# Kernel tuning notes

Measured on AMD Instinct MI355X. Metric: run time of the kernel, lower is better.

Reference implementation:

```python
import jax, jax.numpy as jnp
import numpy as np
from functools import partial

D = 512      # world_state_dim
M = 1000     # memory_size
H = 8        # attention heads
DH = D // H  # head dim
EPS = 1e-5


def _layernorm(x, g, b):
    mu = jnp.mean(x, axis=-1, keepdims=True)
    var = jnp.mean((x - mu) ** 2, axis=-1, keepdims=True)
    return (x - mu) * jax.lax.rsqrt(var + EPS) * g + b


def setup_inputs() -> dict:
    key = jax.random.key(0)
    ks = jax.random.split(key, 24)
    B = 8192
    w = lambda k, shp: (jax.random.normal(k, shp, dtype=jnp.float32) * 0.02)
    inp = {
        "observations": jax.random.normal(ks[0], (B, D), dtype=jnp.float32),
        "ego_motion": jax.random.normal(ks[1], (B, 16), dtype=jnp.float32),
        "world_memory": jax.random.normal(ks[2], (M, D), dtype=jnp.float32) * 0.1,
        # encoder: Linear(D,D) -> ReLU -> LN(D) -> Linear(D,D)
        "enc_w1": w(ks[3], (D, D)), "enc_b1": jnp.zeros((D,), jnp.float32),
        "enc_g": jnp.ones((D,), jnp.float32), "enc_beta": jnp.zeros((D,), jnp.float32),
        "enc_w2": w(ks[4], (D, D)), "enc_b2": jnp.zeros((D,), jnp.float32),
        # multihead attention in/out projections
        "wq": w(ks[5], (D, D)), "bq": jnp.zeros((D,), jnp.float32),
        "wk": w(ks[6], (D, D)), "bk": jnp.zeros((D,), jnp.float32),
        "wv": w(ks[7], (D, D)), "bv": jnp.zeros((D,), jnp.float32),
        "wo": w(ks[8], (D, D)), "bo": jnp.zeros((D,), jnp.float32),
        # transition: Linear(D+16,D) -> ReLU -> LN(D) -> Linear(D,D)
        "tr_w1": w(ks[9], (D, D + 16)), "tr_b1": jnp.zeros((D,), jnp.float32),
        "tr_g": jnp.ones((D,), jnp.float32), "tr_beta": jnp.zeros((D,), jnp.float32),
        "tr_w2": w(ks[10], (D, D)), "tr_b2": jnp.zeros((D,), jnp.float32),
        # quality head: Linear(D,128) -> ReLU -> Linear(128,1) -> Sigmoid
        "q_w1": w(ks[11], (128, D)), "q_b1": jnp.zeros((128,), jnp.float32),
        "q_w2": w(ks[12], (1, 128)), "q_b2": jnp.zeros((1,), jnp.float32),
        # random slots for memory-bank scatter-EMA update (replaces torch.randint)
        "update_indices": jax.random.randint(ks[13], (B,), 0, M, dtype=jnp.int32),
    }
    return inp


def _forward_core(observations, ego_motion, world_memory,
                  enc_w1, enc_b1, enc_g, enc_beta, enc_w2, enc_b2,
                  wq, bq, wk, bk, wv, bv, wo, bo,
                  tr_w1, tr_b1, tr_g, tr_beta, tr_w2, tr_b2,
                  q_w1, q_b1, q_w2, q_b2):
    B = observations.shape[0]
    # world_encoder
    h = jax.nn.relu(observations @ enc_w1.T + enc_b1)
    encoded = _layernorm(h, enc_g, enc_beta) @ enc_w2.T + enc_b2  # [B, D]
    # cross-attention: one query per batch row over shared memory bank
    q = (encoded @ wq.T + bq).reshape(B, H, DH)
    k = (world_memory @ wk.T + bk).reshape(M, H, DH)  # shared across batch
    v = (world_memory @ wv.T + bv).reshape(M, H, DH)
    scores = jnp.einsum("bhd,mhd->bhm", q, k) / jnp.sqrt(jnp.float32(DH))
    attn = jax.nn.softmax(scores, axis=-1)              # [B, H, M]
    ctx = jnp.einsum("bhm,mhd->bhd", attn, v).reshape(B, D)
    memory_states = ctx @ wo.T + bo
    # fuse + transition
    fused = 0.7 * encoded + 0.3 * memory_states
    x = jnp.concatenate([fused, ego_motion], axis=-1)   # [B, D+16]
    h2 = jax.nn.relu(x @ tr_w1.T + tr_b1)
    next_state = _layernorm(h2, tr_g, tr_beta) @ tr_w2.T + tr_b2  # [B, D]
    # quality head
    qh = jax.nn.relu(next_state @ q_w1.T + q_b1)
    quality = jax.nn.sigmoid(qh @ q_w2.T + q_b2)        # [B, 1]
    mem_weights = jnp.mean(attn, axis=1)                # [B, M] avg over heads
    return next_state, quality, mem_weights


def _update_memory_bank(world_memory, next_state, quality, update_indices):
    # Sequential scatter-EMA, faithful to the torch loop (duplicates compound).
    mask = quality[:, 0] > 0.7

    def step(mem, inp):
        idx, st, m = inp
        row = mem[idx]
        new_row = jnp.where(m, 0.9 * row + 0.1 * st, row)
        return mem.at[idx].set(new_row), None

    updated, _ = jax.lax.scan(step, world_memory, (update_indices, next_state, mask))
    return updated


@jax.jit
def reference(observations, ego_motion, world_memory,
              enc_w1, enc_b1, enc_g, enc_beta, enc_w2, enc_b2,
              wq, bq, wk, bk, wv, bv, wo, bo,
              tr_w1, tr_b1, tr_g, tr_beta, tr_w2, tr_b2,
              q_w1, q_b1, q_w2, q_b2, update_indices):
    next_state, quality, mem_weights = _forward_core(
        observations, ego_motion, world_memory,
        enc_w1, enc_b1, enc_g, enc_beta, enc_w2, enc_b2,
        wq, bq, wk, bk, wv, bv, wo, bo,
        tr_w1, tr_b1, tr_g, tr_beta, tr_w2, tr_b2,
        q_w1, q_b1, q_w2, q_b2)
    updated_memory = _update_memory_bank(world_memory, next_state, quality, update_indices)
    return next_state, quality, updated_memory
```

## Files before the change

kernel.cpp:

```cpp
#include <hip/hip_runtime.h>

#define B_ 8192
#define D_ 512
#define M_ 1000
#define H_ 8
#define LOG2E 1.4426950408889634f

typedef unsigned short u16;
typedef __attribute__((ext_vector_type(8))) short bf16x8;
typedef __attribute__((ext_vector_type(4))) float f32x4;

__device__ __forceinline__ float bf2f(u16 u) {
    union { unsigned u; float f; } c; c.u = ((unsigned)u) << 16; return c.f;
}
__device__ __forceinline__ u16 f2bf(float f) {
    union { float f; unsigned u; } c; c.f = f;
    unsigned r = (c.u + 0x7fffu + ((c.u >> 16) & 1u)) >> 16;
    return (u16)r;
}
__device__ __forceinline__ unsigned f2bf_fast_u(float f) {
    union { float f; unsigned u; } c; c.f = f;
    return (c.u + 0x8000u) >> 16;
}
__device__ __forceinline__ float wave_sum(float v) {
#pragma unroll
    for (int off = 32; off > 0; off >>= 1) v += __shfl_xor(v, off);
    return v;
}

template<bool RELU, bool WF32, bool VTOUT>
__device__ __forceinline__ void gemm_core(
    int bx, int by, u16* As, u16* Bs,
    const u16* __restrict__ A0, const u16* __restrict__ A1,
    const u16* __restrict__ A2, int lda0, int lda1, int lda2,
    const u16* __restrict__ W0, const u16* __restrict__ W1,
    const u16* __restrict__ W2, int ldw0, int ldw1, int ldw2,
    int kb1, int kb2,
    const float* __restrict__ bias, float bscale, float cscale,
    float* __restrict__ Cf, u16* __restrict__ Cb, u16* __restrict__ VT,
    int M, int N, int K, int ldc)
{
    const int m0 = by * 64, n0 = bx * 64;
    if (m0 >= M || n0 >= N) return;
    const int t = threadIdx.x, w = t >> 6, l = t & 63;
    const int wm = (w >> 1) * 32, wn = (w & 1) * 32;
    const int li = l & 15, quad = l >> 4;

    f32x4 acc[2][2];
#pragma unroll
    for (int i = 0; i < 2; ++i)
#pragma unroll
        for (int j = 0; j < 2; ++j) acc[i][j] = (f32x4){0.f, 0.f, 0.f, 0.f};

    for (int k0 = 0; k0 < K; k0 += 64) {
        const u16* Ab; const u16* Wb; int ldab, ldwb, ko;
        if (k0 < kb1)      { Ab = A0; ldab = lda0; Wb = W0; ldwb = ldw0; ko = k0; }
        else if (k0 < kb2) { Ab = A1; ldab = lda1; Wb = W1; ldwb = ldw1; ko = k0 - kb1; }
        else               { Ab = A2; ldab = lda2; Wb = W2; ldwb = ldw2; ko = k0 - kb2; }
#pragma unroll
        for (int i = 0; i < 2; ++i) {
            const int rl = w * 16 + i * 8 + (l >> 3);
            const int ck = (l & 7) ^ (rl & 7);
            int ga = m0 + rl; ga = ga < M ? ga : M - 1;
            __builtin_amdgcn_global_load_lds(
                (const __attribute__((address_space(1))) void*)(Ab + (size_t)ga * ldab + ko + ck * 8),
                (__attribute__((address_space(3))) void*)(As + (w * 16 + i * 8) * 64),
                16, 0, 0);
        }
#pragma unroll
        for (int i = 0; i < 2; ++i) {
            const int rl = w * 16 + i * 8 + (l >> 3);
            const int ck = (l & 7) ^ (rl & 7);
            int gb = n0 + rl; gb = gb < N ? gb : N - 1;
            __builtin_amdgcn_global_load_lds(
                (const __attribute__((address_space(1))) void*)(Wb + (size_t)gb * ldwb + ko + ck * 8),
                (__attribute__((address_space(3))) void*)(Bs + (w * 16 + i * 8) * 64),
                16, 0, 0);
        }
        __syncthreads();
#pragma unroll
        for (int ks = 0; ks < 2; ++ks) {
            const int ch = ks * 4 + quad;
            bf16x8 af[2], bfr[2];
#pragma unroll
            for (int mt = 0; mt < 2; ++mt) {
                const int r = wm + mt * 16 + li;
                af[mt] = *(const bf16x8*)(As + r * 64 + ((ch ^ (r & 7)) * 8));
            }
#pragma unroll
            for (int nt = 0; nt < 2; ++nt) {
                const int r = wn + nt * 16 + li;
                bfr[nt] = *(const bf16x8*)(Bs + r * 64 + ((ch ^ (r & 7)) * 8));
            }
#pragma unroll
            for (int mt = 0; mt < 2; ++mt)
#pragma unroll
                for (int nt = 0; nt < 2; ++nt)
                    acc[mt][nt] = __builtin_amdgcn_mfma_f32_16x16x32_bf16(
                        af[mt], bfr[nt], acc[mt][nt], 0, 0, 0);
        }
        __syncthreads();
    }

    float bv[2];
#pragma unroll
    for (int nt = 0; nt < 2; ++nt) bv[nt] = bias[n0 + wn + nt * 16 + li] * bscale;
#pragma unroll
    for (int mt = 0; mt < 2; ++mt) {
        const int row0 = m0 + wm + mt * 16 + quad * 4;
#pragma unroll
        for (int nt = 0; nt < 2; ++nt) {
            const int col = n0 + wn + nt * 16 + li;
            if (VTOUT && col >= 512) {
                ushort4 pk;
                u16 pv[4];
#pragma unroll
                for (int r = 0; r < 4; ++r) {
                    float v = acc[mt][nt][r] * cscale + bv[nt];
                    pv[r] = (row0 + r < M_) ? f2bf(v) : (u16)0;
                }
                pk.x = pv[0]; pk.y = pv[1]; pk.z = pv[2]; pk.w = pv[3];
                *(ushort4*)(VT + (size_t)(col - 512) * 1024 + row0) = pk;
            } else {
#pragma unroll
                for (int r = 0; r < 4; ++r) {
                    const int row = row0 + r;
                    if (row >= M) continue;
                    float v = acc[mt][nt][r] * cscale + bv[nt];
                    if (RELU) v = fmaxf(v, 0.f);
                    Cb[(size_t)row * ldc + col] = f2bf(v);
                    if (WF32) Cf[(size_t)row * ldc + col] = v;
                }
            }
        }
    }
}

template<bool RELU, bool WF32>
__launch_bounds__(256)
__global__ void mgemm(const u16* __restrict__ A0, const u16* __restrict__ A1,
                      const u16* __restrict__ A2, int lda0, int lda1, int lda2,
                      const u16* __restrict__ W0, const u16* __restrict__ W1,
                      const u16* __restrict__ W2, int ldw0, int ldw1, int ldw2,
                      int kb1, int kb2,
                      const float* __restrict__ bias, float bscale, float cscale,
                      float* __restrict__ Cf, u16* __restrict__ Cb,
                      int M, int N, int K, int ldc)
{
    __shared__ u16 As[64 * 64];
    __shared__ u16 Bs[64 * 64];
    gemm_core<RELU, WF32, false>(blockIdx.x, blockIdx.y, As, Bs,
                                 A0, A1, A2, lda0, lda1, lda2,
                                 W0, W1, W2, ldw0, ldw1, ldw2, kb1, kb2,
                                 bias, bscale, cscale, Cf, Cb, nullptr, M, N, K, ldc);
}

__launch_bounds__(256)
__global__ void megagemm(const u16* __restrict__ obs_bf, const u16* __restrict__ w_enc1,
                         const float* __restrict__ enc_b1, u16* __restrict__ hbuf,
                         const u16* __restrict__ wmem_bf, const u16* __restrict__ w_k,
                         const float* __restrict__ bkv, u16* __restrict__ KVbuf,
                         u16* __restrict__ VTb,
                         const u16* __restrict__ w_q, const u16* __restrict__ w_tr1,
                         const u16* __restrict__ w_e2t, const u16* __restrict__ w_wot,
                         u16* __restrict__ w_qe, u16* __restrict__ w_ae,
                         u16* __restrict__ w_co)
{
    __shared__ u16 As[64 * 64];
    __shared__ u16 Bs[64 * 64];
    const int bx = blockIdx.x, by = blockIdx.y;
    if (blockIdx.z == 0) {
        gemm_core<true, false, false>(bx, by, As, Bs,
            obs_bf, obs_bf, obs_bf, 512, 512, 512,
            w_enc1, w_enc1, w_enc1, 512, 512, 512, 512, 512,
            enc_b1, 1.f, 1.f, nullptr, hbuf, nullptr, B_, 512, 512, 512);
    } else {
        if (by < 16) {
            gemm_core<false, false, true>(bx, by, As, Bs,
                wmem_bf, wmem_bf, wmem_bf, 512, 512, 512,
                w_k, w_k, w_k, 512, 512, 512, 512, 512,
                bkv, 1.f, 1.f, nullptr, KVbuf, VTb, 1024, 1024, 512, 1024);
        } else if (by < 24) {
            gemm_core<false, false, false>(bx, by - 16, As, Bs,
                w_q, w_q, w_q, 512, 512, 512,
                w_e2t, w_e2t, w_e2t, 512, 512, 512, 512, 512,
                bkv, 0.f, 1.0f, nullptr, w_qe, nullptr, 512, 512, 512, 512);
        } else if (by < 32) {
            gemm_core<false, false, false>(bx, by - 24, As, Bs,
                w_tr1, w_tr1, w_tr1, 576, 576, 576,
                w_e2t, w_e2t, w_e2t, 512, 512, 512, 512, 512,
                bkv, 0.f, 0.7f, nullptr, w_ae, nullptr, 512, 512, 512, 512);
        } else if (by < 40) {
            gemm_core<false, false, false>(bx, by - 32, As, Bs,
                w_tr1, w_tr1, w_tr1, 576, 576, 576,
                w_wot, w_wot, w_wot, 512, 512, 512, 512, 512,
                bkv, 0.f, 0.3f, nullptr, w_co, nullptr, 512, 512, 512, 512);
        }
    }
}

#define PADK 72

__launch_bounds__(256, 3)
__global__ void attn_kernel(const u16* __restrict__ Q, const u16* __restrict__ KV,
                            const u16* __restrict__ VT, u16* __restrict__ ctx)
{
    __shared__ u16 Ks[2][64 * 64];
    __shared__ u16 Vs[2][64 * 64];
    __shared__ u16 P[4 * 32 * PADK];
    const int t = threadIdx.x, w = t >> 6, l = t & 63;
    const int h = blockIdx.y;
    const int q0 = blockIdx.x * 128 + w * 32;
    u16* Pw = P + w * (32 * PADK);
    const int li = l & 15, quad = l >> 4;

    bf16x8 aq[2][2];
#pragma unroll
    for (int qnt = 0; qnt < 2; ++qnt)
#pragma unroll
        for (int ks = 0; ks < 2; ++ks) {
            const int row = q0 + qnt * 16 + li;
            aq[qnt][ks] = *(const bf16x8*)(Q + (size_t)row * 512 + h * 64 + ks * 32 + quad * 8);
        }

    bf16x8 ones;
#pragma unroll
    for (int i = 0; i < 8; ++i) ones[i] = (short)0x3F80;

    f32x4 oacc[2][4];
    f32x4 lacc[2];
#pragma unroll
    for (int mt = 0; mt < 2; ++mt) {
        lacc[mt] = (f32x4){0.f, 0.f, 0.f, 0.f};
#pragma unroll
        for (int nt = 0; nt < 4; ++nt) oacc[mt][nt] = (f32x4){0.f, 0.f, 0.f, 0.f};
    }

    auto stage = [&](int kc, int buf) {
#pragma unroll
        for (int i = 0; i < 2; ++i) {
            const int f = i * 256 + t;
            const int r = f >> 3;
            const int ck = (f & 7) ^ (r & 7);
            __builtin_amdgcn_global_load_lds(
                (const __attribute__((address_space(1))) void*)(KV + (size_t)(kc + r) * 1024 + h * 64 + ck * 8),
                (__attribute__((address_space(3))) void*)(&Ks[buf][f * 8]),
                16, 0, 0);
        }
#pragma unroll
        for (int i = 0; i < 2; ++i) {
            const int f = i * 256 + t;
            const int r = f >> 3;
            const int ck = (f & 7) ^ (r & 7);
            __builtin_amdgcn_global_load_lds(
                (const __attribute__((address_space(1))) void*)(VT + (size_t)(h * 64 + r) * 1024 + kc + ck * 8),
                (__attribute__((address_space(3))) void*)(&Vs[buf][f * 8]),
                16, 0, 0);
        }
    };

    stage(0, 0);
    for (int ic = 0; ic < 16; ++ic) {
        const int kc = ic * 64;
        __syncthreads();
        if (ic < 15) stage(kc + 64, (ic + 1) & 1);
        const u16* ksb = &Ks[ic & 1][0];
        const u16* vsb = &Vs[ic & 1][0];

        f32x4 s[4][2];
#pragma unroll
        for (int kmt = 0; kmt < 4; ++kmt)
#pragma unroll
            for (int qnt = 0; qnt < 2; ++qnt) s[kmt][qnt] = (f32x4){0.f, 0.f, 0.f, 0.f};
#pragma unroll
        for (int ks = 0; ks < 2; ++ks) {
            const int ch = ks * 4 + quad;
            bf16x8 bk[4];
#pragma unroll
            for (int kmt = 0; kmt < 4; ++kmt) {
                const int key = kmt * 16 + li;
                bk[kmt] = *(const bf16x8*)(ksb + key * 64 + ((ch ^ (key & 7)) * 8));
            }
#pragma unroll
            for (int kmt = 0; kmt < 4; ++kmt)
#pragma unroll
                for (int qnt = 0; qnt < 2; ++qnt)
                    s[kmt][qnt] = __builtin_amdgcn_mfma_f32_16x16x32_bf16(
                        bk[kmt], aq[qnt][ks], s[kmt][qnt], 0, 0, 0);
        }
        if (kc == 960) {
#pragma unroll
            for (int kmt = 2; kmt < 4; ++kmt)
#pragma unroll
                for (int r = 0; r < 4; ++r) {
                    const int key_local = kmt * 16 + quad * 4 + r;
                    if (960 + key_local >= M_) {
                        s[kmt][0][r] = -3.0e38f;
                        s[kmt][1][r] = -3.0e38f;
                    }
                }
        }
#pragma unroll
        for (int kmt = 0; kmt < 4; ++kmt)
#pragma unroll
            for (int qnt = 0; qnt < 2; ++qnt) {
                const unsigned b0 = f2bf_fast_u(exp2f(s[kmt][qnt][0]));
                const unsigned b1 = f2bf_fast_u(exp2f(s[kmt][qnt][1]));
                const unsigned b2w = f2bf_fast_u(exp2f(s[kmt][qnt][2]));
                const unsigned b3 = f2bf_fast_u(exp2f(s[kmt][qnt][3]));
                const int off = (qnt * 16 + li) * PADK + kmt * 16 + quad * 4;
                *(uint2*)(Pw + off) = make_uint2(b0 | (b1 << 16), b2w | (b3 << 16));
            }
#pragma unroll
        for (int ks = 0; ks < 2; ++ks) {
            const int ch = ks * 4 + quad;
            bf16x8 ap[2];
#pragma unroll
            for (int mt = 0; mt < 2; ++mt)
                ap[mt] = *(const bf16x8*)(Pw + (mt * 16 + li) * PADK + ch * 8);
#pragma unroll
            for (int mt = 0; mt < 2; ++mt)
                lacc[mt] = __builtin_amdgcn_mfma_f32_16x16x32_bf16(
                    ap[mt], ones, lacc[mt], 0, 0, 0);
#pragma unroll
            for (int nt = 0; nt < 4; ++nt) {
                const int dh = nt * 16 + li;
                const bf16x8 bvv = *(const bf16x8*)(vsb + dh * 64 + ((ch ^ (dh & 7)) * 8));
#pragma unroll
                for (int mt = 0; mt < 2; ++mt)
                    oacc[mt][nt] = __builtin_amdgcn_mfma_f32_16x16x32_bf16(
                        ap[mt], bvv, oacc[mt][nt], 0, 0, 0);
            }
        }
    }

#pragma unroll
    for (int mt = 0; mt < 2; ++mt)
#pragma unroll
        for (int r = 0; r < 4; ++r) {
            const int row = q0 + mt * 16 + quad * 4 + r;
            const float inv = 1.0f / lacc[mt][r];
#pragma unroll
            for (int nt = 0; nt < 4; ++nt)
                ctx[(size_t)row * 512 + h * 64 + nt * 16 + li] = f2bf(oacc[mt][nt][r] * inv);
        }
}

__launch_bounds__(256)
__global__ void ln_bf(u16* __restrict__ X, const float* __restrict__ g,
                      const float* __restrict__ be, int rows)
{
    const int row = blockIdx.x * 4 + (threadIdx.x >> 6);
    const int lane = threadIdx.x & 63;
    if (row >= rows) return;
    u16* p = X + (size_t)row * 512 + lane * 8;
    uint4 d = *(const uint4*)p;
    const unsigned dd[4] = {d.x, d.y, d.z, d.w};
    float v[8];
#pragma unroll
    for (int i = 0; i < 4; ++i) {
        v[2 * i]     = bf2f((u16)(dd[i] & 0xffffu));
        v[2 * i + 1] = bf2f((u16)(dd[i] >> 16));
    }
    float s = 0.f;
#pragma unroll
    for (int i = 0; i < 8; ++i) s += v[i];
    s = wave_sum(s);
    const float mu = s * (1.0f / 512.0f);
    float vs = 0.f;
#pragma unroll
    for (int i = 0; i < 8; ++i) { v[i] -= mu; vs += v[i] * v[i]; }
    vs = wave_sum(vs);
    const float r = rsqrtf(vs * (1.0f / 512.0f) + 1e-5f);
    const float* gp = g + lane * 8;
    const float* bp = be + lane * 8;
    unsigned o[4];
#pragma unroll
    for (int i = 0; i < 4; ++i) {
        const u16 lo = f2bf(v[2 * i] * r * gp[2 * i] + bp[2 * i]);
        const u16 hi = f2bf(v[2 * i + 1] * r * gp[2 * i + 1] + bp[2 * i + 1]);
        o[i] = (unsigned)lo | ((unsigned)hi << 16);
    }
    *(uint4*)p = make_uint4(o[0], o[1], o[2], o[3]);
}

__launch_bounds__(256)
__global__ void prep_all(const float* enc_w1, const float* wk_f, const float* wv_f,
                         const float* tr_w2, const float* q_w1, const float* wq,
                         const float* tr_w1, const float* enc_w2, const float* wo,
                         const float* obs, const float* wmem, const float* ego,
                         const float* bk, const float* bvv, const float* bq,
                         const float* enc_b2, const float* trb1, const float* bo,
                         u16* w_enc1, u16* w_k, u16* w_v, u16* w_tr2, u16* w_qh,
                         u16* w_q, u16* w_tr1, u16* w_e2t, u16* w_wot,
                         u16* obs_bf, u16* wmem_bf, u16* ego64,
                         float* bkv, float* bqe, float* btr)
{
    __shared__ float tl[64][65];
    const int seg = blockIdx.y;
    const int t = threadIdx.x;
    const int bx = blockIdx.x;

    if (seg <= 5) {
        const float* s; u16* d; int n; float sc = 1.0f;
        switch (seg) {
            case 0: s = enc_w1; d = w_enc1; n = 262144; break;
            case 1: s = wk_f;   d = w_k;    n = 262144; break;
            case 2: s = wv_f;   d = w_v;    n = 262144; break;
            case 3: s = tr_w2;  d = w_tr2;  n = 262144; break;
            case 4: s = q_w1;   d = w_qh;   n = 65536;  break;
            default: s = wq;    d = w_q;    n = 262144; sc = 0.125f * LOG2E; break;
        }
        const int i0 = (bx * 256 + t) * 4;
        if (i0 + 3 < n) {
            const float4 v = *(const float4*)(s + i0);
            ushort4 o;
            o.x = f2bf(v.x * sc); o.y = f2bf(v.y * sc);
            o.z = f2bf(v.z * sc); o.w = f2bf(v.w * sc);
            *(ushort4*)(d + i0) = o;
        }
    } else if (seg == 6) {
#pragma unroll
        for (int k = 0; k < 4; ++k) {
            const int i = (bx * 256 + t) * 4 + k;
            if (i < 294912) {
                const int r = i / 576, c = i - r * 576;
                w_tr1[i] = (c < 528) ? f2bf(tr_w1[r * 528 + c]) : (u16)0;
            }
        }
    } else if (seg <= 8) {
        if (bx >= 64) return;
        const float* S = (seg == 7) ? enc_w2 : wo;
        u16* D = (seg == 7) ? w_e2t : w_wot;
        const int r0 = (bx >> 3) * 64, c0 = (bx & 7) * 64;
#pragma unroll
        for (int i = 0; i < 16; ++i) {
            const int idx = t + i * 256;
            tl[idx >> 6][idx & 63] = S[(size_t)(r0 + (idx >> 6)) * 512 + c0 + (idx & 63)];
        }
        __syncthreads();
#pragma unroll
        for (int i = 0; i < 16; ++i) {
            const int idx = t + i * 256;
            const int c = idx >> 6, r = idx & 63;
            D[(size_t)(c0 + c) * 512 + r0 + r] = f2bf(tl[r][c]);
        }
    } else if (seg == 9) {
        const int nth = gridDim.x * 256;
        for (int i = bx * 256 + t; i < B_ * 512 / 4; i += nth) {
            const float4 v = ((const float4*)obs)[i];
            ushort4 o;
            o.x = f2bf(v.x); o.y = f2bf(v.y); o.z = f2bf(v.z); o.w = f2bf(v.w);
            ((ushort4*)obs_bf)[i] = o;
        }
    } else if (seg == 10) {
        const int nth = gridDim.x * 256;
        for (int i = bx * 256 + t; i < M_ * 512 / 4; i += nth) {
            const float4 v = ((const float4*)wmem)[i];
            ushort4 o;
            o.x = f2bf(v.x); o.y = f2bf(v.y); o.z = f2bf(v.z); o.w = f2bf(v.w);
            ((ushort4*)wmem_bf)[i] = o;
        }
    } else if (seg == 11) {
        const int nth = gridDim.x * 256;
        for (int i = bx * 256 + t; i < B_ * 64; i += nth) {
            const int b = i >> 6, j = i & 63;
            ego64[(size_t)b * 64 + j] = (j < 16) ? f2bf(ego[b * 16 + j]) : (u16)0;
        }
        const int tid = bx * 256 + t;
        if (tid < 1024) bkv[tid] = (tid < 512) ? bk[tid] : bvv[tid - 512];
    } else {
        if (bx >= 128) return;
        const int i = bx * 4 + (t >> 6);
        const int lane = t & 63;
        float s = 0.f;
        if (seg == 12) {
            const float* wr = wq + (size_t)i * 512 + lane * 8;
#pragma unroll
            for (int j = 0; j < 8; ++j) s += wr[j] * enc_b2[lane * 8 + j];
            s = wave_sum(s);
            if (lane == 0) bqe[i] = 0.125f * LOG2E * (bq[i] + s);
        } else {
            const float* wr = tr_w1 + (size_t)i * 528 + lane * 8;
#pragma unroll
            for (int j = 0; j < 8; ++j)
                s += wr[j] * (0.7f * enc_b2[lane * 8 + j] + 0.3f * bo[lane * 8 + j]);
            s = wave_sum(s);
            if (lane == 0) btr[i] = trb1[i] + s;
        }
    }
}

__global__ void quality_bf(const u16* __restrict__ qh, const float* __restrict__ w2,
                           const float* __restrict__ b2, float* __restrict__ outq,
                           int rows)
{
    const int row = blockIdx.x * 4 + (threadIdx.x >> 6);
    const int lane = threadIdx.x & 63;
    if (row >= rows) return;
    const u16* p = qh + (size_t)row * 128;
    float s = bf2f(p[lane]) * w2[lane] + bf2f(p[64 + lane]) * w2[64 + lane];
    s = wave_sum(s);
    if (lane == 0) outq[row] = 1.0f / (1.0f + expf(-(s + b2[0])));
}

__global__ void compact_kernel(const float* __restrict__ q,
                               int* __restrict__ list, int* __restrict__ cnt)
{
    __shared__ int wtot[16];
    __shared__ int sbase;
    const int t = threadIdx.x, w = t >> 6, lane = t & 63;
    if (t == 0) sbase = 0;
    __syncthreads();
    for (int c = 0; c < B_; c += 1024) {
        const int idx = c + t;
        const bool pred = (q[idx] > 0.7f);
        const unsigned long long bal = __ballot(pred);
        const int prefix = __popcll(bal & ((1ull << lane) - 1ull));
        if (lane == 0) wtot[w] = __popcll(bal);
        __syncthreads();
        int woff = 0;
        for (int i = 0; i < w; ++i) woff += wtot[i];
        if (pred) list[sbase + woff + prefix] = idx;
        __syncthreads();
        if (t == 0) {
            int tot = 0;
            for (int i = 0; i < 16; ++i) tot += wtot[i];
            sbase += tot;
        }
        __syncthreads();
    }
    if (t == 0) *cnt = sbase;
}

__global__ void update_memory_kernel(const float* __restrict__ mem,
                                     const float* __restrict__ ns,
                                     const int* __restrict__ upd,
                                     const int* __restrict__ list,
                                     const int* __restrict__ cnt,
                                     float* __restrict__ outmem)
{
    const int m = blockIdx.x;
    const int t = threadIdx.x;
    const int c4 = t * 4;
    float4 r = *(const float4*)(mem + (size_t)m * D_ + c4);
    const int n = *cnt;
    for (int i = 0; i < n; ++i) {
        const int b = list[i];
        if (upd[b] == m) {
            const float4 s = *(const float4*)(ns + (size_t)b * D_ + c4);
            r.x = 0.9f * r.x + 0.1f * s.x;
            r.y = 0.9f * r.y + 0.1f * s.y;
            r.z = 0.9f * r.z + 0.1f * s.z;
            r.w = 0.9f * r.w + 0.1f * s.w;
        }
    }
    *(float4*)(outmem + (size_t)m * D_ + c4) = r;
}

extern "C" void kernel_launch(void* const* d_in, const int* in_sizes, int n_in,
                              void* d_out, int out_size, void* d_ws, size_t ws_size,
                              hipStream_t stream)
{
    const float* obs    = (const float*)d_in[0];
    const float* ego    = (const float*)d_in[1];
    const float* wmem   = (const float*)d_in[2];
    const float* enc_w1 = (const float*)d_in[3];
    const float* enc_b1 = (const float*)d_in[4];
    const float* enc_g  = (const float*)d_in[5];
    const float* enc_be = (const float*)d_in[6];
    const float* enc_w2 = (const float*)d_in[7];
    const float* enc_b2 = (const float*)d_in[8];
    const float* wq = (const float*)d_in[9];
    const float* bq = (const float*)d_in[10];
    const float* wk_f = (const float*)d_in[11];
    const float* bk = (const float*)d_in[12];
    const float* wv_f = (const float*)d_in[13];
    const float* bvv = (const float*)d_in[14];
    const float* wo = (const float*)d_in[15];
    const float* bo = (const float*)d_in[16];
    const float* tr_w1 = (const float*)d_in[17];
    const float* tr_b1 = (const float*)d_in[18];
    const float* tr_g  = (const float*)d_in[19];
    const float* tr_be = (const float*)d_in[20];
    const float* tr_w2 = (const float*)d_in[21];
    const float* tr_b2 = (const float*)d_in[22];
    const float* q_w1 = (const float*)d_in[23];
    const float* q_b1 = (const float*)d_in[24];
    const float* q_w2 = (const float*)d_in[25];
    const float* q_b2 = (const float*)d_in[26];
    const int*   upd  = (const int*)d_in[27];

    float* out_ns  = (float*)d_out;
    float* out_q   = out_ns + (size_t)B_ * D_;
    float* out_mem = out_q + B_;

    u16* ws = (u16*)d_ws;
    size_t o = 0;
    u16* obs_bf  = ws + o; o += (size_t)B_ * 512;
    u16* wmem_bf = ws + o; o += (size_t)M_ * 512;
    u16* w_enc1  = ws + o; o += 262144;
    u16* w_k     = ws + o; o += 262144;
    u16* w_v     = ws + o; o += 262144;
    u16* w_tr2   = ws + o; o += 262144;
    u16* w_qh    = ws + o; o += 65536;
    u16* w_q     = ws + o; o += 262144;
    u16* w_tr1   = ws + o; o += (size_t)512 * 576;
    u16* w_e2t   = ws + o; o += 262144;
    u16* w_wot   = ws + o; o += 262144;
    u16* w_qe    = ws + o; o += 262144;
    u16* w_ae    = ws + o; o += 262144;
    u16* w_co    = ws + o; o += 262144;
    u16* hbuf    = ws + o; o += (size_t)B_ * 512;
    u16* qbuf    = ws + o; o += (size_t)B_ * 512;
    u16* KVbuf   = ws + o; o += (size_t)1024 * 1024;
    u16* VTb     = ws + o; o += (size_t)512 * 1024;
    u16* ctx     = ws + o; o += (size_t)B_ * 512;
    u16* h2b     = ws + o; o += (size_t)B_ * 512;
    u16* nsbf    = ws + o; o += (size_t)B_ * 512;
    u16* qhb     = ws + o; o += (size_t)B_ * 128;
    u16* ego64   = ws + o; o += (size_t)B_ * 64;
    float* bkv   = (float*)(ws + o); o += 2048;
    float* bqe   = (float*)(ws + o); o += 1024;
    float* btr   = (float*)(ws + o); o += 1024;
    int* list    = (int*)(ws + o);
    int* cnt     = list + B_;

    const dim3 blk(256);

    prep_all<<<dim3(576, 14), blk, 0, stream>>>(
        enc_w1, wk_f, wv_f, tr_w2, q_w1, wq, tr_w1, enc_w2, wo,
        obs, wmem, ego, bk, bvv, bq, enc_b2, tr_b1, bo,
        w_enc1, w_k, w_v, w_tr2, w_qh, w_q, w_tr1, w_e2t, w_wot,
        obs_bf, wmem_bf, ego64, bkv, bqe, btr);

    megagemm<<<dim3(16, 128, 2), blk, 0, stream>>>(
        obs_bf, w_enc1, enc_b1, hbuf, wmem_bf, w_k, bkv, KVbuf, VTb,
        w_q, w_tr1, w_e2t, w_wot, w_qe, w_ae, w_co);

    ln_bf<<<dim3(2048), blk, 0, stream>>>(hbuf, enc_g, enc_be, B_);

    mgemm<false, false><<<dim3(8, 128), blk, 0, stream>>>(
        hbuf, hbuf, hbuf, 512, 512, 512, w_qe, w_qe, w_qe, 512, 512, 512,
        512, 512, bqe, 1.f, 1.f, nullptr, qbuf, B_, 512, 512, 512);

    attn_kernel<<<dim3(64, 8), blk, 0, stream>>>(qbuf, KVbuf, VTb, ctx);

    mgemm<true, false><<<dim3(8, 128), blk, 0, stream>>>(
        hbuf, ctx, ego64, 512, 512, 64, w_ae, w_co, w_tr1 + 512, 512, 512, 576,
        512, 1024, btr, 1.f, 1.f, nullptr, h2b, B_, 512, 1088, 512);
    ln_bf<<<dim3(2048), blk, 0, stream>>>(h2b, tr_g, tr_be, B_);

    mgemm<false, true><<<dim3(8, 128), blk, 0, stream>>>(
        h2b, h2b, h2b, 512, 512, 512, w_tr2, w_tr2, w_tr2, 512, 512, 512,
        512, 512, tr_b2, 1.f, 1.f, out_ns, nsbf, B_, 512, 512, 512);

    mgemm<true, false><<<dim3(2, 128), blk, 0, stream>>>(
        nsbf, nsbf, nsbf, 512, 512, 512, w_qh, w_qh, w_qh, 512, 512, 512,
        512, 512, q_b1, 1.f, 1.f, nullptr, qhb, B_, 128, 512, 128);
    quality_bf<<<dim3(2048), blk, 0, stream>>>(qhb, q_w2, q_b2, out_q, B_);

    compact_kernel<<<dim3(1), dim3(1024), 0, stream>>>(out_q, list, cnt);
    update_memory_kernel<<<dim3(M_), dim3(128), 0, stream>>>(
        wmem, out_ns, upd, list, cnt, out_mem);
}
```

Baseline: 264.9 us.

## Double-buffer GEMM LDS tiles with K=32 steps and prefetch next stage

Restructures the shared GEMM core's K loop from 64-wide single-buffered tiles with two barriers per step into 32-wide double-buffered tiles. The global-to-LDS load of the next step is issued before computing the current one, leaving one barrier per step. The aim is to overlap memory latency with MFMA work. In exchange it doubles the number of loop iterations, uses a new swizzle, and relies on a single barrier to protect buffer reuse, which is a possible race if loads are still in flight.

```diff
diff --git a/kernel.cpp b/kernel.cpp
--- a/kernel.cpp
+++ b/kernel.cpp
@@ -46,60 +46,59 @@
     const int wm = (w >> 1) * 32, wn = (w & 1) * 32;
     const int li = l & 15, quad = l >> 4;
 
+    const int srow = t >> 2;
+    const int scol = ((t & 3) ^ ((t >> 3) & 3)) * 8;
+    int gaA = m0 + srow; gaA = gaA < M ? gaA : M - 1;
+    int gbB = n0 + srow; gbB = gbB < N ? gbB : N - 1;
+
     f32x4 acc[2][2];
 #pragma unroll
     for (int i = 0; i < 2; ++i)
 #pragma unroll
         for (int j = 0; j < 2; ++j) acc[i][j] = (f32x4){0.f, 0.f, 0.f, 0.f};
 
-    for (int k0 = 0; k0 < K; k0 += 64) {
+    const int nsteps = K >> 5;
+
+    auto stage = [&](int step, int buf) {
+        const int k0 = step * 32;
         const u16* Ab; const u16* Wb; int ldab, ldwb, ko;
         if (k0 < kb1)      { Ab = A0; ldab = lda0; Wb = W0; ldwb = ldw0; ko = k0; }
         else if (k0 < kb2) { Ab = A1; ldab = lda1; Wb = W1; ldwb = ldw1; ko = k0 - kb1; }
         else               { Ab = A2; ldab = lda2; Wb = W2; ldwb = ldw2; ko = k0 - kb2; }
-#pragma unroll
-        for (int i = 0; i < 2; ++i) {
-            const int rl = w * 16 + i * 8 + (l >> 3);
-            const int ck = (l & 7) ^ (rl & 7);
-            int ga = m0 + rl; ga = ga < M ? ga : M - 1;
-            __builtin_amdgcn_global_load_lds(
-                (const __attribute__((address_space(1))) void*)(Ab + (size_t)ga * ldab + ko + ck * 8),
-                (__attribute__((address_space(3))) void*)(As + (w * 16 + i * 8) * 64),
-                16, 0, 0);
-        }
-#pragma unroll
-        for (int i = 0; i < 2; ++i) {
-            const int rl = w * 16 + i * 8 + (l >> 3);
-            const int ck = (l & 7) ^ (rl & 7);
-            int gb = n0 + rl; gb = gb < N ? gb : N - 1;
-            __builtin_amdgcn_global_load_lds(
-                (const __attribute__((address_space(1))) void*)(Wb + (size_t)gb * ldwb + ko + ck * 8),
-                (__attribute__((address_space(3))) void*)(Bs + (w * 16 + i * 8) * 64),
-                16, 0, 0);
-        }
+        __builtin_amdgcn_global_load_lds(
+            (const __attribute__((address_space(1))) void*)(Ab + (size_t)gaA * ldab + ko + scol),
+            (__attribute__((address_space(3))) void*)(As + buf * 2048 + w * 512),
+            16, 0, 0);
+        __builtin_amdgcn_global_load_lds(
+            (const __attribute__((address_space(1))) void*)(Wb + (size_t)gbB * ldwb + ko + scol),
+            (__attribute__((address_space(3))) void*)(Bs + buf * 2048 + w * 512),
+            16, 0, 0);
+    };
+
+    stage(0, 0);
+    const int sw = (li >> 1) & 3;
+    for (int step = 0; step < nsteps; ++step) {
         __syncthreads();
-#pragma unroll
-        for (int ks = 0; ks < 2; ++ks) {
-            const int ch = ks * 4 + quad;
-            bf16x8 af[2], bfr[2];
-#pragma unroll
-            for (int mt = 0; mt < 2; ++mt) {
-                const int r = wm + mt * 16 + li;
-                af[mt] = *(const bf16x8*)(As + r * 64 + ((ch ^ (r & 7)) * 8));
-            }
-#pragma unroll
-            for (int nt = 0; nt < 2; ++nt) {
-                const int r = wn + nt * 16 + li;
-                bfr[nt] = *(const bf16x8*)(Bs + r * 64 + ((ch ^ (r & 7)) * 8));
-            }
-#pragma unroll
-            for (int mt = 0; mt < 2; ++mt)
-#pragma unroll
-                for (int nt = 0; nt < 2; ++nt)
-                    acc[mt][nt] = __builtin_amdgcn_mfma_f32_16x16x32_bf16(
-                        af[mt], bfr[nt], acc[mt][nt], 0, 0, 0);
-        }
-        __syncthreads();
+        if (step + 1 < nsteps) stage(step + 1, (step + 1) & 1);
+        const u16* as = As + (step & 1) * 2048;
+        const u16* bs = Bs + (step & 1) * 2048;
+        bf16x8 af[2], bfr[2];
+#pragma unroll
+        for (int mt = 0; mt < 2; ++mt) {
+            const int r = wm + mt * 16 + li;
+            af[mt] = *(const bf16x8*)(as + r * 32 + ((quad ^ sw) * 8));
+        }
+#pragma unroll
+        for (int nt = 0; nt < 2; ++nt) {
+            const int r = wn + nt * 16 + li;
+            bfr[nt] = *(const bf16x8*)(bs + r * 32 + ((quad ^ sw) * 8));
+        }
+#pragma unroll
+        for (int mt = 0; mt < 2; ++mt)
+#pragma unroll
+            for (int nt = 0; nt < 2; ++nt)
+                acc[mt][nt] = __builtin_amdgcn_mfma_f32_16x16x32_bf16(
+                    af[mt], bfr[nt], acc[mt][nt], 0, 0, 0);
     }
 
     float bv[2];
@@ -147,8 +146,8 @@
                       float* __restrict__ Cf, u16* __restrict__ Cb,
                       int M, int N, int K, int ldc)
 {
-    __shared__ u16 As[64 * 64];
-    __shared__ u16 Bs[64 * 64];
+    __shared__ u16 As[2 * 2048];
+    __shared__ u16 Bs[2 * 2048];
     gemm_core<RELU, WF32, false>(blockIdx.x, blockIdx.y, As, Bs,
                                  A0, A1, A2, lda0, lda1, lda2,
                                  W0, W1, W2, ldw0, ldw1, ldw2, kb1, kb2,
@@ -166,8 +165,8 @@
                          u16* __restrict__ w_qe, u16* __restrict__ w_ae,
                          u16* __restrict__ w_co)
 {
-    __shared__ u16 As[64 * 64];
-    __shared__ u16 Bs[64 * 64];
+    __shared__ u16 As[2 * 2048];
+    __shared__ u16 Bs[2 * 2048];
     const int bx = blockIdx.x, by = blockIdx.y;
     if (blockIdx.z == 0) {
         gemm_core<true, false, false>(bx, by, As, Bs,
```

New measurement: 279.7 us. 1.06x slower.
